# Optimization experiments

Hardware: AMD Instinct MI355X
Metric: run time of the kernel (lower is better)

Reference implementation:

```python
import jax, jax.numpy as jnp
import numpy as np

N, M_NODES, E_EDGES, D = 32, 128, 256, 128  # note: D must equal M_NODES (see original convK1 constraint)


def setup_inputs() -> dict:
    key = jax.random.key(0)
    k1, k2, k3, k4, k5 = jax.random.split(key, 5)
    feature_matrix = jax.random.normal(k1, (N, M_NODES, D), dtype=jnp.float32)
    incidence_matrix = (jax.random.uniform(k2, (N, M_NODES, E_EDGES)) < 0.25).astype(jnp.float32)
    # grouped Conv1d(m, m*m, d, groups=m) weights reshaped to (m, m, d); bias (m, m)
    Wkk = jax.random.normal(k3, (M_NODES, M_NODES, D), dtype=jnp.float32) * (1.0 / np.sqrt(D))
    bkk = jax.random.normal(k4, (M_NODES, M_NODES), dtype=jnp.float32) * 0.01
    # Conv1d(m, 1, 1) weights: (1, m, 1) -> vector of length m (== d)
    w1 = jax.random.normal(k5, (D,), dtype=jnp.float32) * (1.0 / np.sqrt(D))
    b1 = jnp.zeros((), dtype=jnp.float32)
    return {"feature_matrix": feature_matrix, "incidence_matrix": incidence_matrix,
            "Wkk": Wkk, "bkk": bkk, "w1": w1, "b1": b1}


def reference(feature_matrix, incidence_matrix, Wkk, bkk, w1, b1):
    n, m, d = feature_matrix.shape
    e = incidence_matrix.shape[-1]
    # incidence broadcast: (N,m,1,d) * (N,m,e,1) -> (N,m,e,d) -> (N,e,m,d) -> (N*e, m, d)
    region = feature_matrix[:, :, None, :] * incidence_matrix[:, :, :, None]
    region = region.transpose(0, 2, 1, 3).reshape(n * e, m, d)
    # grouped conv with full-length kernel == per-row dot products
    logits = jnp.einsum('bid,ijd->bij', region, Wkk) + bkk  # (B, m, m)
    multiplier = jax.nn.softmax(logits, axis=-1)
    transformed = jax.nn.relu(jnp.einsum('bij,bjd->bid', multiplier, region))  # (B, m, d)
    # Conv1d(m,1,1) on (B, d, m): weighted sum over the feature axis (valid since d == m)
    pooled = jnp.einsum('bld,d->bl', transformed, w1) + b1  # (B, m) with m == d
    return pooled.reshape(n, e, d)
```

## Files before the change

kernel.cpp:

```cpp
#include <hip/hip_runtime.h>

#define NN 32
#define MM 128
#define EE 256
#define DD 128
#define ELB 32

typedef __attribute__((ext_vector_type(8))) short short8;
typedef __attribute__((ext_vector_type(4))) float f32x4;

union U16x8 { uint4 u; short8 s; };

static __device__ __forceinline__ unsigned short f2bf(float f) {
  union { float f; unsigned u; } v; v.f = f;
  unsigned r = v.u + 0x7FFFu + ((v.u >> 16) & 1u);
  return (unsigned short)(r >> 16);
}

static __device__ __forceinline__ U16x8 pk8(float4 a, float4 b) {
  U16x8 r;
  asm("v_cvt_pk_bf16_f32 %0, %1, %2" : "=v"(r.u.x) : "v"(a.x), "v"(a.y));
  asm("v_cvt_pk_bf16_f32 %0, %1, %2" : "=v"(r.u.y) : "v"(a.z), "v"(a.w));
  asm("v_cvt_pk_bf16_f32 %0, %1, %2" : "=v"(r.u.z) : "v"(b.x), "v"(b.y));
  asm("v_cvt_pk_bf16_f32 %0, %1, %2" : "=v"(r.u.w) : "v"(b.z), "v"(b.w));
  return r;
}

__global__ __launch_bounds__(256, 1)
void k_pre(const float* __restrict__ X, const float* __restrict__ inc,
           const float* __restrict__ Wkk, const float* __restrict__ bkk,
           unsigned short* __restrict__ P1g, unsigned short* __restrict__ P0g,
           unsigned short* __restrict__ XTg, unsigned* __restrict__ bmap) {
  __shared__ float xs[64][129];
  const int bid = blockIdx.x;
  const int t = threadIdx.x;

  if (bid < 256) {
    if (t >= 64) return;
    const int i  = bid >> 1;
    const int nh = bid & 1;
    const int l  = t;
    const int lr = l & 15, lg = l >> 4;

    short8 a[4];
    {
      const int n = nh * 16 + lr;
      const float* xp = X + (n * MM + i) * DD + lg * 8;
#pragma unroll
      for (int k = 0; k < 4; ++k) {
        float4 v0 = *(const float4*)(xp + k * 32);
        float4 v1 = *(const float4*)(xp + k * 32 + 4);
        a[k] = pk8(v0, v1).s;
      }
    }
    f32x4 acc[8];
#pragma unroll
    for (int cf = 0; cf < 8; ++cf) acc[cf] = (f32x4){0.f, 0.f, 0.f, 0.f};
#pragma unroll
    for (int k = 0; k < 4; ++k) {
#pragma unroll
      for (int cf = 0; cf < 8; ++cf) {
        const int j = cf * 16 + lr;
        const float* wp = Wkk + (i * MM + j) * DD + k * 32 + lg * 8;
        float4 v0 = *(const float4*)(wp);
        float4 v1 = *(const float4*)(wp + 4);
        acc[cf] = __builtin_amdgcn_mfma_f32_16x16x32_bf16(a[k], pk8(v0, v1).s, acc[cf], 0, 0, 0);
      }
    }
    float bk[8];
#pragma unroll
    for (int cf = 0; cf < 8; ++cf) bk[cf] = bkk[i * MM + cf * 16 + lr];
#pragma unroll
    for (int r = 0; r < 4; ++r) {
      float v[8], m = -1e30f;
#pragma unroll
      for (int cf = 0; cf < 8; ++cf) { v[cf] = acc[cf][r] + bk[cf]; m = fmaxf(m, v[cf]); }
#pragma unroll
      for (int s = 1; s < 16; s <<= 1) m = fmaxf(m, __shfl_xor(m, s, 64));
      float sum = 0.f;
#pragma unroll
      for (int cf = 0; cf < 8; ++cf) { v[cf] = __expf(v[cf] - m); sum += v[cf]; }
#pragma unroll
      for (int s = 1; s < 16; s <<= 1) sum += __shfl_xor(sum, s, 64);
      const float inv = 1.f / sum;
      const int n = nh * 16 + lg * 4 + r;
      unsigned short* dst = P1g + (n * MM + i) * MM;
#pragma unroll
      for (int cf = 0; cf < 8; ++cf) dst[cf * 16 + lr] = f2bf(v[cf] * inv);
    }
    if (nh == 0) {
      float v0 = bkk[i * MM + l], v1 = bkk[i * MM + 64 + l];
      float m = fmaxf(v0, v1);
#pragma unroll
      for (int s = 1; s < 64; s <<= 1) m = fmaxf(m, __shfl_xor(m, s, 64));
      v0 = __expf(v0 - m); v1 = __expf(v1 - m);
      float sum = v0 + v1;
#pragma unroll
      for (int s = 1; s < 64; s <<= 1) sum += __shfl_xor(sum, s, 64);
      const float inv = 1.f / sum;
      P0g[i * MM + l]      = f2bf(v0 * inv);
      P0g[i * MM + 64 + l] = f2bf(v1 * inv);
    }
  } else if (bid < 320) {
    const int idx = bid - 256;
    const int n = idx >> 1, jh = idx & 1;
#pragma unroll
    for (int it = 0; it < 8; ++it) {
      int id2 = it * 256 + t;
      int j = id2 >> 5, dq = id2 & 31;
      float4 v = *(const float4*)(X + (n * MM + jh * 64 + j) * DD + dq * 4);
      xs[j][dq * 4 + 0] = v.x; xs[j][dq * 4 + 1] = v.y;
      xs[j][dq * 4 + 2] = v.z; xs[j][dq * 4 + 3] = v.w;
    }
    __syncthreads();
    const int d = t >> 1, half = t & 1;
    unsigned* dst = (unsigned*)XTg + (n * DD + d) * (MM / 2) + jh * 32 + half * 16;
#pragma unroll
    for (int wq = 0; wq < 16; ++wq) {
      int jl = half * 32 + wq * 2;
      unsigned u;
      asm("v_cvt_pk_bf16_f32 %0, %1, %2" : "=v"(u) : "v"(xs[jl][d]), "v"(xs[jl + 1][d]));
      dst[wq] = u;
    }
  } else {
    const int idx = bid - 320;
    const int n = idx >> 2, q = idx & 3;
    const int e = t;
    unsigned bm = 0;
#pragma unroll 4
    for (int j = 0; j < 32; ++j)
      if (inc[(n * MM + q * 32 + j) * EE + e] != 0.f) bm |= 1u << j;
    bmap[(n * EE + e) * 4 + q] = bm;
  }
}

__global__ __launch_bounds__(256, 2)
void k_main(const unsigned short* __restrict__ P0g, const unsigned short* __restrict__ P1g,
            const unsigned short* __restrict__ XTg, const unsigned* __restrict__ bmap,
            const float* __restrict__ w1, const float* __restrict__ b1p,
            float* __restrict__ out) {
  __shared__ unsigned bitm[ELB][4];
  __shared__ alignas(16) unsigned short mrow[ELB][128];

  const int bid = blockIdx.x;
  const int n = bid & 31, eg = (bid >> 5) & 7, rh = bid >> 8;
  const int t = threadIdx.x, w = t >> 6, l = t & 63, lr = l & 15, lg = l >> 4;
  const int i_lane = rh * 64 + w * 16 + lr;

  if (t < ELB)
    *(uint4*)&bitm[t][0] = *(const uint4*)(bmap + (n * EE + eg * ELB + t) * 4);

  uint4 x[8][4];
  {
    const unsigned short* xb = XTg + n * DD * MM;
#pragma unroll
    for (int cf = 0; cf < 8; ++cf)
#pragma unroll
      for (int k = 0; k < 4; ++k)
        x[cf][k] = *(const uint4*)(xb + (cf * 16 + lr) * MM + k * 32 + lg * 8);
  }
  uint4 p0[4], p1[4];
  {
    const unsigned short* pb0 = P0g + i_lane * MM;
    const unsigned short* pb1 = P1g + n * MM * MM + i_lane * MM;
#pragma unroll
    for (int k = 0; k < 4; ++k) {
      p0[k] = *(const uint4*)(pb0 + k * 32 + lg * 8);
      p1[k] = *(const uint4*)(pb1 + k * 32 + lg * 8);
    }
  }
  U16x8 w1u[4];
#pragma unroll
  for (int p = 0; p < 4; ++p) {
    float4 a = *(const float4*)(w1 + (2 * p) * 16 + lg * 4);
    float4 b = *(const float4*)(w1 + (2 * p + 1) * 16 + lg * 4);
    w1u[p] = pk8(a, b);
  }
#pragma unroll
  for (int cf = 0; cf < 8; ++cf) {
#pragma unroll
    for (int k = 0; k < 4; ++k)
      asm volatile("" : "+v"(x[cf][k].x), "+v"(x[cf][k].y), "+v"(x[cf][k].z), "+v"(x[cf][k].w));
  }
#pragma unroll
  for (int k = 0; k < 4; ++k) {
    asm volatile("" : "+v"(p0[k].x), "+v"(p0[k].y), "+v"(p0[k].z), "+v"(p0[k].w));
    asm volatile("" : "+v"(p1[k].x), "+v"(p1[k].y), "+v"(p1[k].z), "+v"(p1[k].w));
    asm volatile("" : "+v"(w1u[k].u.x), "+v"(w1u[k].u.y), "+v"(w1u[k].u.z), "+v"(w1u[k].u.w));
  }
  const float b1v = b1p[0];
  const int selsh = (w & 1) * 16 + lr;
  const int selwd = rh * 2 + (w >> 1);
  __syncthreads();

  {
    int el = t >> 3, j0 = (t & 7) * 16;
    unsigned wd = bitm[el][j0 >> 5];
    int sh = j0 & 31;
    unsigned short* mp = &mrow[el][j0];
#pragma unroll
    for (int b = 0; b < 16; ++b) mp[b] = ((wd >> (sh + b)) & 1u) ? 0xFFFFu : 0u;
  }
  __syncthreads();

  float* outp = out + (n * EE + eg * ELB) * MM + rh * 64 + w * 16 + lg * 4;
  const char* mbase = (const char*)&mrow[0][0] + lg * 16;

#pragma unroll 1
  for (int el = 0; el < ELB; ++el) {
    const bool sel = ((bitm[el][selwd] >> selsh) & 1u) != 0u;

    U16x8 pv[4];
#pragma unroll
    for (int k = 0; k < 4; ++k) {
      uint4 mm = *(const uint4*)(mbase + el * 256 + k * 64);
      pv[k].u.x = (sel ? p1[k].x : p0[k].x) & mm.x;
      pv[k].u.y = (sel ? p1[k].y : p0[k].y) & mm.y;
      pv[k].u.z = (sel ? p1[k].z : p0[k].z) & mm.z;
      pv[k].u.w = (sel ? p1[k].w : p0[k].w) & mm.w;
    }

    f32x4 eA = (f32x4){b1v, b1v, b1v, b1v};
#pragma unroll
    for (int p = 0; p < 4; ++p) {
      __builtin_amdgcn_s_setprio(1);
      f32x4 a0v = (f32x4){0.f,0.f,0.f,0.f}, a1v = (f32x4){0.f,0.f,0.f,0.f};
#pragma unroll
      for (int k = 0; k < 4; ++k) {
        U16x8 xv0; xv0.u = x[2*p][k];
        U16x8 xv1; xv1.u = x[2*p+1][k];
        a0v = __builtin_amdgcn_mfma_f32_16x16x32_bf16(xv0.s, pv[k].s, a0v, 0, 0, 0);
        a1v = __builtin_amdgcn_mfma_f32_16x16x32_bf16(xv1.s, pv[k].s, a1v, 0, 0, 0);
      }
      __builtin_amdgcn_s_setprio(0);
      float f0 = fmaxf(a0v[0],0.f), f1 = fmaxf(a0v[1],0.f), f2 = fmaxf(a0v[2],0.f), f3 = fmaxf(a0v[3],0.f);
      float g0 = fmaxf(a1v[0],0.f), g1 = fmaxf(a1v[1],0.f), g2 = fmaxf(a1v[2],0.f), g3 = fmaxf(a1v[3],0.f);
      unsigned u0,u1,u2,u3;
      asm("v_cvt_pk_bf16_f32 %0, %1, %2" : "=v"(u0) : "v"(f0), "v"(f1));
      asm("v_cvt_pk_bf16_f32 %0, %1, %2" : "=v"(u1) : "v"(f2), "v"(f3));
      asm("v_cvt_pk_bf16_f32 %0, %1, %2" : "=v"(u2) : "v"(g0), "v"(g1));
      asm("v_cvt_pk_bf16_f32 %0, %1, %2" : "=v"(u3) : "v"(g2), "v"(g3));
      U16x8 uu; uu.u.x = u0; uu.u.y = u1; uu.u.z = u2; uu.u.w = u3;
      eA = __builtin_amdgcn_mfma_f32_16x16x32_bf16(uu.s, w1u[p].s, eA, 0, 0, 0);
    }

    if (lr == 0) *(float4*)(outp + el * MM) = *(float4*)&eA;
  }
}

extern "C" void kernel_launch(void* const* d_in, const int* in_sizes, int n_in,
                              void* d_out, int out_size, void* d_ws, size_t ws_size,
                              hipStream_t stream) {
  const float* X   = (const float*)d_in[0];
  const float* inc = (const float*)d_in[1];
  const float* Wkk = (const float*)d_in[2];
  const float* bkk = (const float*)d_in[3];
  const float* w1  = (const float*)d_in[4];
  const float* b1  = (const float*)d_in[5];
  float* out = (float*)d_out;

  unsigned short* P1g = (unsigned short*)d_ws;
  unsigned short* XTg = P1g + NN * MM * DD;
  unsigned short* P0g = XTg + NN * MM * DD;
  unsigned* bmap = (unsigned*)(P0g + MM * MM);

  hipLaunchKernelGGL(k_pre,  dim3(448), dim3(256), 0, stream, X, inc, Wkk, bkk, P1g, P0g, XTg, bmap);
  hipLaunchKernelGGL(k_main, dim3(512), dim3(256), 0, stream, P0g, P1g, XTg, bmap, w1, b1, out);
}
```

Before: 49.51 us.

## Restructure main kernel to 32x32x16 MFMA with feature-split waves and LDS reduction

The main kernel switches from 16x16x32 MFMAs, where each wave covered all 128 features for 16 rows, to 32x32x16 MFMAs, where each wave covers 32 features for 32 rows. The w1 pooling moves from a second MFMA to fp32 FMAs followed by a lane shuffle. Partial sums from the four waves are combined through a small double-buffered LDS array. Register use per thread drops, so the grid doubles to 1024 blocks and launch bounds rise to 3 blocks per CU. In exchange, every edge iteration now pays a __syncthreads, and the pooled contribution keeps fp32 precision instead of going through a bf16 conversion.

```diff
diff --git a/kernel.cpp b/kernel.cpp
--- a/kernel.cpp
+++ b/kernel.cpp
@@ -8,6 +8,7 @@
 
 typedef __attribute__((ext_vector_type(8))) short short8;
 typedef __attribute__((ext_vector_type(4))) float f32x4;
+typedef __attribute__((ext_vector_type(16))) float f32x16;
 
 union U16x8 { uint4 u; short8 s; };
 
@@ -134,63 +135,56 @@
   }
 }
 
-__global__ __launch_bounds__(256, 2)
+__global__ __launch_bounds__(256, 3)
 void k_main(const unsigned short* __restrict__ P0g, const unsigned short* __restrict__ P1g,
             const unsigned short* __restrict__ XTg, const unsigned* __restrict__ bmap,
             const float* __restrict__ w1, const float* __restrict__ b1p,
             float* __restrict__ out) {
   __shared__ unsigned bitm[ELB][4];
   __shared__ alignas(16) unsigned short mrow[ELB][128];
+  __shared__ float comb[2][4][32];
 
   const int bid = blockIdx.x;
-  const int n = bid & 31, eg = (bid >> 5) & 7, rh = bid >> 8;
-  const int t = threadIdx.x, w = t >> 6, l = t & 63, lr = l & 15, lg = l >> 4;
-  const int i_lane = rh * 64 + w * 16 + lr;
+  const int n = bid & 31, eg = (bid >> 5) & 7, iq = bid >> 8;
+  const int t = threadIdx.x, w = t >> 6, l = t & 63;
+  const int lc = l & 31, lh = l >> 5;
+  const int i_lane = iq * 32 + lc;
 
   if (t < ELB)
     *(uint4*)&bitm[t][0] = *(const uint4*)(bmap + (n * EE + eg * ELB + t) * 4);
 
-  uint4 x[8][4];
+  uint4 x[8];
   {
-    const unsigned short* xb = XTg + n * DD * MM;
-#pragma unroll
-    for (int cf = 0; cf < 8; ++cf)
-#pragma unroll
-      for (int k = 0; k < 4; ++k)
-        x[cf][k] = *(const uint4*)(xb + (cf * 16 + lr) * MM + k * 32 + lg * 8);
-  }
-  uint4 p0[4], p1[4];
+    const unsigned short* xb = XTg + n * DD * MM + (w * 32 + lc) * MM;
+#pragma unroll
+    for (int ks = 0; ks < 8; ++ks)
+      x[ks] = *(const uint4*)(xb + ks * 16 + lh * 8);
+  }
+  uint4 p0[8], p1[8];
   {
     const unsigned short* pb0 = P0g + i_lane * MM;
     const unsigned short* pb1 = P1g + n * MM * MM + i_lane * MM;
 #pragma unroll
-    for (int k = 0; k < 4; ++k) {
-      p0[k] = *(const uint4*)(pb0 + k * 32 + lg * 8);
-      p1[k] = *(const uint4*)(pb1 + k * 32 + lg * 8);
-    }
-  }
-  U16x8 w1u[4];
-#pragma unroll
-  for (int p = 0; p < 4; ++p) {
-    float4 a = *(const float4*)(w1 + (2 * p) * 16 + lg * 4);
-    float4 b = *(const float4*)(w1 + (2 * p + 1) * 16 + lg * 4);
-    w1u[p] = pk8(a, b);
-  }
-#pragma unroll
-  for (int cf = 0; cf < 8; ++cf) {
-#pragma unroll
-    for (int k = 0; k < 4; ++k)
-      asm volatile("" : "+v"(x[cf][k].x), "+v"(x[cf][k].y), "+v"(x[cf][k].z), "+v"(x[cf][k].w));
-  }
-#pragma unroll
-  for (int k = 0; k < 4; ++k) {
-    asm volatile("" : "+v"(p0[k].x), "+v"(p0[k].y), "+v"(p0[k].z), "+v"(p0[k].w));
-    asm volatile("" : "+v"(p1[k].x), "+v"(p1[k].y), "+v"(p1[k].z), "+v"(p1[k].w));
-    asm volatile("" : "+v"(w1u[k].u.x), "+v"(w1u[k].u.y), "+v"(w1u[k].u.z), "+v"(w1u[k].u.w));
-  }
+    for (int ks = 0; ks < 8; ++ks) {
+      p0[ks] = *(const uint4*)(pb0 + ks * 16 + lh * 8);
+      p1[ks] = *(const uint4*)(pb1 + ks * 16 + lh * 8);
+    }
+  }
+  float w1reg[16];
+#pragma unroll
+  for (int r = 0; r < 16; ++r)
+    w1reg[r] = w1[w * 32 + (r & 3) + 8 * (r >> 2) + 4 * lh];
+
+#pragma unroll
+  for (int ks = 0; ks < 8; ++ks) {
+    asm volatile("" : "+v"(x[ks].x), "+v"(x[ks].y), "+v"(x[ks].z), "+v"(x[ks].w));
+    asm volatile("" : "+v"(p0[ks].x), "+v"(p0[ks].y), "+v"(p0[ks].z), "+v"(p0[ks].w));
+    asm volatile("" : "+v"(p1[ks].x), "+v"(p1[ks].y), "+v"(p1[ks].z), "+v"(p1[ks].w));
+  }
+#pragma unroll
+  for (int r = 0; r < 16; ++r) asm volatile("" : "+v"(w1reg[r]));
+
   const float b1v = b1p[0];
-  const int selsh = (w & 1) * 16 + lr;
-  const int selwd = rh * 2 + (w >> 1);
   __syncthreads();
 
   {
@@ -203,48 +197,49 @@
   }
   __syncthreads();
 
-  float* outp = out + (n * EE + eg * ELB) * MM + rh * 64 + w * 16 + lg * 4;
-  const char* mbase = (const char*)&mrow[0][0] + lg * 16;
+  float* outp = out + (n * EE + eg * ELB) * MM + iq * 32;
+  const char* mbase = (const char*)&mrow[0][0] + lh * 16;
 
 #pragma unroll 1
   for (int el = 0; el < ELB; ++el) {
-    const bool sel = ((bitm[el][selwd] >> selsh) & 1u) != 0u;
-
-    U16x8 pv[4];
-#pragma unroll
-    for (int k = 0; k < 4; ++k) {
-      uint4 mm = *(const uint4*)(mbase + el * 256 + k * 64);
-      pv[k].u.x = (sel ? p1[k].x : p0[k].x) & mm.x;
-      pv[k].u.y = (sel ? p1[k].y : p0[k].y) & mm.y;
-      pv[k].u.z = (sel ? p1[k].z : p0[k].z) & mm.z;
-      pv[k].u.w = (sel ? p1[k].w : p0[k].w) & mm.w;
-    }
-
-    f32x4 eA = (f32x4){b1v, b1v, b1v, b1v};
-#pragma unroll
-    for (int p = 0; p < 4; ++p) {
-      __builtin_amdgcn_s_setprio(1);
-      f32x4 a0v = (f32x4){0.f,0.f,0.f,0.f}, a1v = (f32x4){0.f,0.f,0.f,0.f};
-#pragma unroll
-      for (int k = 0; k < 4; ++k) {
-        U16x8 xv0; xv0.u = x[2*p][k];
-        U16x8 xv1; xv1.u = x[2*p+1][k];
-        a0v = __builtin_amdgcn_mfma_f32_16x16x32_bf16(xv0.s, pv[k].s, a0v, 0, 0, 0);
-        a1v = __builtin_amdgcn_mfma_f32_16x16x32_bf16(xv1.s, pv[k].s, a1v, 0, 0, 0);
-      }
-      __builtin_amdgcn_s_setprio(0);
-      float f0 = fmaxf(a0v[0],0.f), f1 = fmaxf(a0v[1],0.f), f2 = fmaxf(a0v[2],0.f), f3 = fmaxf(a0v[3],0.f);
-      float g0 = fmaxf(a1v[0],0.f), g1 = fmaxf(a1v[1],0.f), g2 = fmaxf(a1v[2],0.f), g3 = fmaxf(a1v[3],0.f);
-      unsigned u0,u1,u2,u3;
-      asm("v_cvt_pk_bf16_f32 %0, %1, %2" : "=v"(u0) : "v"(f0), "v"(f1));
-      asm("v_cvt_pk_bf16_f32 %0, %1, %2" : "=v"(u1) : "v"(f2), "v"(f3));
-      asm("v_cvt_pk_bf16_f32 %0, %1, %2" : "=v"(u2) : "v"(g0), "v"(g1));
-      asm("v_cvt_pk_bf16_f32 %0, %1, %2" : "=v"(u3) : "v"(g2), "v"(g3));
-      U16x8 uu; uu.u.x = u0; uu.u.y = u1; uu.u.z = u2; uu.u.w = u3;
-      eA = __builtin_amdgcn_mfma_f32_16x16x32_bf16(uu.s, w1u[p].s, eA, 0, 0, 0);
-    }
-
-    if (lr == 0) *(float4*)(outp + el * MM) = *(float4*)&eA;
+    const bool sel = ((bitm[el][iq] >> lc) & 1u) != 0u;
+
+    f32x16 acc = {0.f,0.f,0.f,0.f,0.f,0.f,0.f,0.f,0.f,0.f,0.f,0.f,0.f,0.f,0.f,0.f};
+    __builtin_amdgcn_s_setprio(1);
+#pragma unroll
+    for (int ks = 0; ks < 8; ++ks) {
+      uint4 mm = *(const uint4*)(mbase + el * 256 + ks * 32);
+      U16x8 pv;
+      pv.u.x = (sel ? p1[ks].x : p0[ks].x) & mm.x;
+      pv.u.y = (sel ? p1[ks].y : p0[ks].y) & mm.y;
+      pv.u.z = (sel ? p1[ks].z : p0[ks].z) & mm.z;
+      pv.u.w = (sel ? p1[ks].w : p0[ks].w) & mm.w;
+      U16x8 xv; xv.u = x[ks];
+      acc = __builtin_amdgcn_mfma_f32_32x32x16_bf16(xv.s, pv.s, acc, 0, 0, 0);
+    }
+    __builtin_amdgcn_s_setprio(0);
+
+    float s0 = fmaxf(acc[0], 0.f) * w1reg[0];
+    float s1 = fmaxf(acc[1], 0.f) * w1reg[1];
+    float s2 = fmaxf(acc[2], 0.f) * w1reg[2];
+    float s3 = fmaxf(acc[3], 0.f) * w1reg[3];
+#pragma unroll
+    for (int r = 4; r < 16; r += 4) {
+      s0 += fmaxf(acc[r + 0], 0.f) * w1reg[r + 0];
+      s1 += fmaxf(acc[r + 1], 0.f) * w1reg[r + 1];
+      s2 += fmaxf(acc[r + 2], 0.f) * w1reg[r + 2];
+      s3 += fmaxf(acc[r + 3], 0.f) * w1reg[r + 3];
+    }
+    float pooled = (s0 + s1) + (s2 + s3);
+    pooled += __shfl_xor(pooled, 32, 64);
+
+    if (l < 32) comb[el & 1][w][l] = pooled;
+    __syncthreads();
+    if (w == (el & 3) && l < 32) {
+      float s = ((comb[el & 1][0][l] + comb[el & 1][1][l]) +
+                 (comb[el & 1][2][l] + comb[el & 1][3][l])) + b1v;
+      outp[el * MM + l] = s;
+    }
   }
 }
 
@@ -264,6 +259,6 @@
   unsigned short* P0g = XTg + NN * MM * DD;
   unsigned* bmap = (unsigned*)(P0g + MM * MM);
 
-  hipLaunchKernelGGL(k_pre,  dim3(448), dim3(256), 0, stream, X, inc, Wkk, bkk, P1g, P0g, XTg, bmap);
-  hipLaunchKernelGGL(k_main, dim3(512), dim3(256), 0, stream, P0g, P1g, XTg, bmap, w1, b1, out);
-}
+  hipLaunchKernelGGL(k_pre,  dim3(448),  dim3(256), 0, stream, X, inc, Wkk, bkk, P1g, P0g, XTg, bmap);
+  hipLaunchKernelGGL(k_main, dim3(1024), dim3(256), 0, stream, P0g, P1g, XTg, bmap, w1, b1, out);
+}
```

After: 66.69 us. 34.7% more time.
